# Kernel optimization log

Hardware: AMD Instinct MI355X
Metric: run time of the kernel (lower is better)

The kernel has to match this reference:

```python
import jax, jax.numpy as jnp
import numpy as np

B, C, M, H, K, V, Fdim = 2, 2048, 1024, 16, 64, 64, 4096
EPS = 1e-5


def layer_norm(x, g, b):
    mu = jnp.mean(x, axis=-1, keepdims=True)
    var = jnp.mean((x - mu) ** 2, axis=-1, keepdims=True)
    return (x - mu) * jax.lax.rsqrt(var + EPS) * g + b


def mha(kvinput, qinput, wq, wk, wv, wo, masked):
    # kvinput/qinput: [b,c,m]; wq/wk: [h,m,k]; wv: [h,m,v]; wo: [h,v,m]
    kval = jnp.einsum('bcm,hmk->bhck', kvinput, wk)
    qval = jnp.einsum('bcm,hmk->bhck', qinput, wq)
    vval = jnp.einsum('bcm,hmv->bhcv', kvinput, wv)
    # logits: c indexes keys, d indexes queries (faithful to original)
    alogit = jnp.einsum('bhck,bhdk->bhcd', kval, qval)
    if masked:
        side = alogit.shape[2]
        # triu INCLUDING diagonal, added before scaling (faithful quirk)
        mask = jnp.triu(jnp.full((side, side), -100.0, dtype=alogit.dtype))
        alogit = alogit + mask
    scale = 1.0 / np.sqrt(wq.shape[-1]).astype(np.float32)
    att = jax.nn.softmax(alogit * scale, axis=2)  # normalize over keys c
    pre = jnp.einsum('bhcd,bhcv->bhdv', att, vval)
    return jnp.einsum('bhdv,hvm->bdm', pre, wo)


def setup_inputs() -> dict:
    key = jax.random.key(0)
    ks = jax.random.split(key, 14)
    d = {
        'enc_out': jax.random.normal(ks[0], (B, C, M), jnp.float32),
        'x': jax.random.normal(ks[1], (B, C, M), jnp.float32),
        # masked self-attention params
        'wq1': jax.random.normal(ks[2], (H, M, K), jnp.float32),
        'wk1': jax.random.normal(ks[3], (H, M, K), jnp.float32),
        'wv1': jax.random.normal(ks[4], (H, M, V), jnp.float32),
        'wo1': jax.random.normal(ks[5], (H, V, M), jnp.float32),
        'g1': jnp.ones((M,), jnp.float32), 'b1': jnp.zeros((M,), jnp.float32),
        # cross-attention params
        'wq2': jax.random.normal(ks[6], (H, M, K), jnp.float32),
        'wk2': jax.random.normal(ks[7], (H, M, K), jnp.float32),
        'wv2': jax.random.normal(ks[8], (H, M, V), jnp.float32),
        'wo2': jax.random.normal(ks[9], (H, V, M), jnp.float32),
        'g2': jnp.ones((M,), jnp.float32), 'b2': jnp.zeros((M,), jnp.float32),
        # FFN params
        'fw1': jax.random.normal(ks[10], (M, Fdim), jnp.float32),
        'fb1': jnp.zeros((Fdim,), jnp.float32),
        'fw2': jax.random.normal(ks[11], (Fdim, M), jnp.float32),
        'fb2': jnp.zeros((M,), jnp.float32),
        'g3': jnp.ones((M,), jnp.float32), 'b3': jnp.zeros((M,), jnp.float32),
    }
    return d


def reference(enc_out, x, wq1, wk1, wv1, wo1, g1, b1,
              wq2, wk2, wv2, wo2, g2, b2,
              fw1, fb1, fw2, fb2, g3, b3):
    att1 = mha(x, x, wq1, wk1, wv1, wo1, masked=True)
    n1 = layer_norm(x + att1, g1, b1)
    att2 = mha(enc_out, n1, wq2, wk2, wv2, wo2, masked=False)
    n2 = layer_norm(n1 + att2, g2, b2)
    ff = jnp.einsum('bcf,fm->bcm', jax.nn.relu(jnp.einsum('bcm,mf->bcf', n2, fw1) + fb1), fw2) + fb2
    return layer_norm(n2 + ff, g3, b3)
```

## Files before the change

### kernel.cpp

```cpp
#include <hip/hip_runtime.h>
#include <math.h>

#define B_ 2
#define C_ 2048
#define M_ 1024
#define H_ 16
#define KV_ 64
#define F_ 4096

typedef __attribute__((ext_vector_type(8))) __bf16 bf16x8;
typedef __attribute__((ext_vector_type(4))) float f32x4;
typedef unsigned short u16;

#if defined(__has_builtin)
#if __has_builtin(__builtin_amdgcn_mfma_f64_16x16x4f64)
#define HAVE_MFMA64 1
#endif
#endif
#ifndef HAVE_MFMA64
#define HAVE_MFMA64 0
#endif

#if HAVE_MFMA64
typedef __attribute__((ext_vector_type(4))) double f64x4;
#endif

__device__ __forceinline__ float bf2f(u16 u) {
    union { unsigned int i; float f; } x; x.i = ((unsigned int)u) << 16; return x.f;
}
__device__ __forceinline__ u16 f2bf(float f) {
    union { float f; unsigned int i; } x; x.f = f;
    unsigned int r = x.i + 0x7fffu + ((x.i >> 16) & 1u);
    return (u16)(r >> 16);
}
__device__ __forceinline__ float ldflag(const void* p, size_t i, int isf) {
    return isf ? ((const float*)p)[i] : bf2f(((const u16*)p)[i]);
}

__device__ __forceinline__ double blockReduceSumD(double v, double* red, int tid) {
#pragma unroll
    for (int off = 32; off > 0; off >>= 1) v += __shfl_down(v, off, 64);
    if ((tid & 63) == 0) red[tid >> 6] = v;
    __syncthreads();
    v = red[0] + red[1] + red[2] + red[3];
    __syncthreads();
    return v;
}

__global__ void detect_dtype(const unsigned int* __restrict__ w, int* __restrict__ flags) {
    __shared__ int cnt[256];
    int t = threadIdx.x, c = 0;
    for (int i = t; i < 2048; i += 256) {
        unsigned int e = (w[i] >> 7) & 0xffu;
        if (e >= 140u || (e > 0u && e < 91u)) c++;
    }
    cnt[t] = c; __syncthreads();
    for (int s = 128; s > 0; s >>= 1) { if (t < s) cnt[t] += cnt[t + s]; __syncthreads(); }
    if (t == 0) flags[0] = (cnt[0] > 300) ? 1 : 0;
}

__device__ __forceinline__ float sAval(int m, int k) { return (float)(((m * 5 + k * 3) % 7) - 3); }
__device__ __forceinline__ float sBval(int k, int n) { return (float)(((k * 11 + n * 2) % 5) - 2); }
__device__ __forceinline__ float sQval(int m, int k) { return (float)(((m * 3 + k * 7) % 9) - 4); }
__device__ __forceinline__ float sKval(int c, int k) { return (float)(((c * 5 + k * 2) % 8) - 3); }

__global__ __launch_bounds__(256) void calibrate(int* __restrict__ cal) {
#if HAVE_MFMA64
    __shared__ int ctab[64][12];
    __shared__ int s_ok, s_bad;
    __shared__ float Ast[32][65], Bs[32][65];
    __shared__ float Qv[64][65], Kv[64][65];
    const int t = threadIdx.x;
    if (t == 0) { s_ok = 0; s_bad = 0; }
    __syncthreads();
    if (t < 64) {
        const int l = t;
        f64x4 z = {0.0, 0.0, 0.0, 0.0};
        f64x4 p1 = __builtin_amdgcn_mfma_f64_16x16x4f64(1.0, (double)l, z, 0, 0, 0);
        f64x4 p2 = __builtin_amdgcn_mfma_f64_16x16x4f64((double)l, 1.0, z, 0, 0, 0);
        int ok = 1, bFam = 0, aFam = 0;
        int colD[4], rowD[4];
#pragma unroll
        for (int r = 0; r < 4; r++) {
            double pv = p1[r];
            int f = 0, n = 0;
            if (pv >= 0.0 && pv <= 4096.0) {
                long long vi = (long long)(pv + 0.5);
                if (vi >= 96 && vi <= 156 && ((vi - 96) & 3) == 0) { f = 1; n = (int)((vi - 96) >> 2); }
                else if (vi >= 6 && vi <= 246 && ((vi - 6) & 15) == 0) { f = 2; n = (int)((vi - 6) >> 4); }
            }
            if (f == 0) ok = 0;
            if (r == 0) bFam = f; else if (f != bFam) ok = 0;
            colD[r] = n;
            pv = p2[r]; f = 0; n = 0;
            if (pv >= 0.0 && pv <= 4096.0) {
                long long wi = (long long)(pv + 0.5);
                if (wi >= 96 && wi <= 156 && ((wi - 96) & 3) == 0) { f = 1; n = (int)((wi - 96) >> 2); }
                else if (wi >= 6 && wi <= 246 && ((wi - 6) & 15) == 0) { f = 2; n = (int)((wi - 6) >> 4); }
            }
            if (f == 0) ok = 0;
            if (r == 0) aFam = f; else if (f != aFam) ok = 0;
            rowD[r] = n;
        }
        if (colD[1] != colD[0] || colD[2] != colD[0] || colD[3] != colD[0]) ok = 0;
        int rm = (1 << rowD[0]) | (1 << rowD[1]) | (1 << rowD[2]) | (1 << rowD[3]);
        if (__popc(rm) != 4) ok = 0;
        int cm = 1 << colD[0];
#pragma unroll
        for (int off = 1; off < 16; off <<= 1) {
#pragma unroll
            for (int r = 0; r < 4; r++)
                if (__shfl_xor(rowD[r], off, 64) != rowD[r]) ok = 0;
            cm |= __shfl_xor(cm, off, 64);
        }
        if (cm != 0xffff) ok = 0;
        const int am = (aFam == 2) ? (l >> 2) : (l & 15);
        const int ak = (aFam == 2) ? (l & 3) : (l >> 4);
        const int bn = (bFam == 2) ? (l >> 2) : (l & 15);
        const int bk = (bFam == 2) ? (l & 3) : (l >> 4);
        {
            double a3 = (double)sAval(am, ak);
            double b3 = (double)sBval(bk, bn);
            f64x4 p3 = __builtin_amdgcn_mfma_f64_16x16x4f64(a3, b3, z, 0, 0, 0);
#pragma unroll
            for (int r = 0; r < 4; r++) {
                double ref = 0.0;
                for (int k2 = 0; k2 < 4; k2++)
                    ref += (double)sAval(rowD[r], k2) * (double)sBval(k2, colD[0]);
                if (p3[r] != ref) ok = 0;
            }
        }
        unsigned long long bb = __ballot(ok != 0);
        ctab[l][0] = am; ctab[l][1] = ak; ctab[l][2] = bn; ctab[l][3] = bk;
        ctab[l][4] = colD[0];
        ctab[l][5] = rowD[0]; ctab[l][6] = rowD[1]; ctab[l][7] = rowD[2]; ctab[l][8] = rowD[3];
        ctab[l][9] = 0; ctab[l][10] = 0; ctab[l][11] = 0;
        if (l == 0) s_ok = (bb == ~0ull) ? 1 : 0;
    }
    __syncthreads();
    for (int i = t; i < 32 * 64; i += 256) {
        int k2 = i >> 6, m2 = i & 63;
        Ast[k2][m2] = sAval(m2, k2);
        Bs[k2][m2] = sBval(k2, m2);
    }
    for (int i = t; i < 64 * 64; i += 256) {
        int r2 = i >> 6, c2 = i & 63;
        Qv[r2][c2] = sQval(r2, c2);
        Kv[r2][c2] = sKval(r2, c2);
    }
    __syncthreads();
    if (s_ok) {
        const int w = t >> 6;
        const int* cl = ctab[t & 63];
        const int am = cl[0], ak2 = cl[1], bn2 = cl[2], bk2 = cl[3], cD = cl[4];
        const int rd[4] = {cl[5], cl[6], cl[7], cl[8]};
        int ok = 1;
        {
            f64x4 acc4[4] = { {0,0,0,0},{0,0,0,0},{0,0,0,0},{0,0,0,0} };
#pragma unroll
            for (int ks = 0; ks < 8; ks++) {
                double ad = (double)Ast[4 * ks + ak2][16 * w + am];
#pragma unroll
                for (int nt = 0; nt < 4; nt++) {
                    double bd = (double)Bs[4 * ks + bk2][16 * nt + bn2];
                    acc4[nt] = __builtin_amdgcn_mfma_f64_16x16x4f64(ad, bd, acc4[nt], 0, 0, 0);
                }
            }
#pragma unroll
            for (int nt = 0; nt < 4; nt++)
#pragma unroll
                for (int i = 0; i < 4; i++) {
                    int row = 16 * w + rd[i], col = 16 * nt + cD;
                    double ref = 0.0;
                    for (int k2 = 0; k2 < 32; k2++)
                        ref += (double)sAval(row, k2) * (double)sBval(k2, col);
                    if (acc4[nt][i] != ref) ok = 0;
                }
        }
        {
            double aqv[16];
#pragma unroll
            for (int ks = 0; ks < 16; ks++)
                aqv[ks] = (double)Qv[16 * w + am][4 * ks + ak2];
            f64x4 S[4] = { {0,0,0,0},{0,0,0,0},{0,0,0,0},{0,0,0,0} };
#pragma unroll
            for (int ks = 0; ks < 16; ks++) {
#pragma unroll
                for (int nt = 0; nt < 4; nt++) {
                    double bd = (double)Kv[16 * nt + bn2][4 * ks + bk2];
                    S[nt] = __builtin_amdgcn_mfma_f64_16x16x4f64(aqv[ks], bd, S[nt], 0, 0, 0);
                }
            }
#pragma unroll
            for (int nt = 0; nt < 4; nt++)
#pragma unroll
                for (int i = 0; i < 4; i++) {
                    int row = 16 * w + rd[i], col = 16 * nt + cD;
                    double ref = 0.0;
                    for (int k2 = 0; k2 < 64; k2++)
                        ref += (double)sQval(row, k2) * (double)sKval(col, k2);
                    if (S[nt][i] != ref) ok = 0;
                }
        }
        if (!ok) s_bad = 1;
    }
    __syncthreads();
    if (t < 64) {
#pragma unroll
        for (int j = 0; j < 12; j++) cal[16 + t * 12 + j] = ctab[t][j];
    }
    if (t == 0) cal[0] = (s_ok && !s_bad) ? 1 : 0;
#else
    if (threadIdx.x == 0) cal[0] = 0;
#endif
}

__global__ __launch_bounds__(256) void v_to_bf16t(
    const float* __restrict__ vv, u16* __restrict__ hi, u16* __restrict__ lo)
{
    __shared__ float Ls[64][65];
    const int bh = blockIdx.y, c0 = blockIdx.x * 64;
    const int t = threadIdx.x;
    const int c = t >> 2, vb = (t & 3) * 16;
    const float* src = vv + ((size_t)bh * C_ + c0 + c) * KV_ + vb;
#pragma unroll
    for (int i = 0; i < 4; i++) {
        float4 p = *(const float4*)(src + 4 * i);
        Ls[vb + 4*i + 0][c] = p.x;
        Ls[vb + 4*i + 1][c] = p.y;
        Ls[vb + 4*i + 2][c] = p.z;
        Ls[vb + 4*i + 3][c] = p.w;
    }
    __syncthreads();
#pragma unroll
    for (int it = 0; it < 2; it++) {
        int idx = t + 256 * it;
        int v = idx >> 3, ch = idx & 7;
        u16 h8[8], l8[8];
#pragma unroll
        for (int j = 0; j < 8; j++) {
            float x = Ls[v][ch * 8 + j];
            h8[j] = f2bf(x);
            l8[j] = f2bf(x - bf2f(h8[j]));
        }
        size_t off = ((size_t)bh * KV_ + v) * C_ + c0 + ch * 8;
        int4 hp, lp;
        hp.x = (int)((unsigned)h8[0] | ((unsigned)h8[1] << 16));
        hp.y = (int)((unsigned)h8[2] | ((unsigned)h8[3] << 16));
        hp.z = (int)((unsigned)h8[4] | ((unsigned)h8[5] << 16));
        hp.w = (int)((unsigned)h8[6] | ((unsigned)h8[7] << 16));
        lp.x = (int)((unsigned)l8[0] | ((unsigned)l8[1] << 16));
        lp.y = (int)((unsigned)l8[2] | ((unsigned)l8[3] << 16));
        lp.z = (int)((unsigned)l8[4] | ((unsigned)l8[5] << 16));
        lp.w = (int)((unsigned)l8[6] | ((unsigned)l8[7] << 16));
        *(int4*)(hi + off) = hp;
        *(int4*)(lo + off) = lp;
    }
}

template<int AMODE>
__global__ __launch_bounds__(256) void proj_qk64(
    const void* __restrict__ Ab, const void* __restrict__ Bb,
    float* __restrict__ Cb, const int* __restrict__ flags,
    const int* __restrict__ cal,
    int N, int Kd, long long a_bstr, long long b_hstr, long long c_zstr, int NH)
{
    const int isf = flags[0];
    const int isfA = (AMODE == 1) ? 1 : isf;
    __shared__ float Ast[32][65];
    __shared__ float Bs[32][65];
    const int t = threadIdx.x;
    const int m0 = blockIdx.x * 64, n0 = blockIdx.y * 64;
    const int zb = blockIdx.z / NH, zh = blockIdx.z % NH;
    const size_t aoff = (size_t)zb * a_bstr, boff = (size_t)zh * b_hstr;
    const size_t czoff = (size_t)blockIdx.z * c_zstr;
    const int ar = t >> 2, ak = (t & 3) * 8;
    const int bk = t >> 3, bn = (t & 7) * 8;
    const int cok = cal[0];

#if HAVE_MFMA64
    if (cok) {
        const int* cl = cal + 16 + (t & 63) * 12;
        const int am = cl[0], ak2 = cl[1], bn2 = cl[2], bk2 = cl[3], cD = cl[4];
        const int rd[4] = {cl[5], cl[6], cl[7], cl[8]};
        const int w = t >> 6;
        f64x4 acc4[4] = { {0,0,0,0},{0,0,0,0},{0,0,0,0},{0,0,0,0} };
        for (int k0 = 0; k0 < Kd; k0 += 32) {
            float av[8];
            {
                size_t off = aoff + (size_t)(m0 + ar) * Kd + k0 + ak;
                if (isfA) {
                    const float* ap = (const float*)Ab + off;
                    float4 p0 = *(const float4*)ap, p1 = *((const float4*)ap + 1);
                    av[0]=p0.x; av[1]=p0.y; av[2]=p0.z; av[3]=p0.w;
                    av[4]=p1.x; av[5]=p1.y; av[6]=p1.z; av[7]=p1.w;
                } else {
                    const u16* ap = (const u16*)Ab + off;
                    int4 p = *(const int4*)ap;
                    unsigned int u[4] = {(unsigned)p.x,(unsigned)p.y,(unsigned)p.z,(unsigned)p.w};
#pragma unroll
                    for (int j = 0; j < 4; j++) {
                        av[2*j]   = bf2f((u16)(u[j] & 0xffffu));
                        av[2*j+1] = bf2f((u16)(u[j] >> 16));
                    }
                }
            }
#pragma unroll
            for (int j = 0; j < 8; j++) Ast[ak + j][ar] = av[j];
            float bv[8];
            {
                size_t off = boff + (size_t)(k0 + bk) * N + n0 + bn;
                if (isf) {
                    const float* bp = (const float*)Bb + off;
                    float4 p0 = *(const float4*)bp, p1 = *((const float4*)bp + 1);
                    bv[0]=p0.x; bv[1]=p0.y; bv[2]=p0.z; bv[3]=p0.w;
                    bv[4]=p1.x; bv[5]=p1.y; bv[6]=p1.z; bv[7]=p1.w;
                } else {
                    const u16* bp = (const u16*)Bb + off;
                    int4 p = *(const int4*)bp;
                    unsigned int u[4] = {(unsigned)p.x,(unsigned)p.y,(unsigned)p.z,(unsigned)p.w};
#pragma unroll
                    for (int j = 0; j < 4; j++) {
                        bv[2*j]   = bf2f((u16)(u[j] & 0xffffu));
                        bv[2*j+1] = bf2f((u16)(u[j] >> 16));
                    }
                }
            }
#pragma unroll
            for (int j = 0; j < 8; j++) Bs[bk][bn + j] = bv[j];
            __syncthreads();
#pragma unroll
            for (int ks = 0; ks < 8; ks++) {
                double ad = (double)Ast[4 * ks + ak2][16 * w + am];
#pragma unroll
                for (int nt = 0; nt < 4; nt++) {
                    double bd = (double)Bs[4 * ks + bk2][16 * nt + bn2];
                    acc4[nt] = __builtin_amdgcn_mfma_f64_16x16x4f64(ad, bd, acc4[nt], 0, 0, 0);
                }
            }
            __syncthreads();
        }
#pragma unroll
        for (int nt = 0; nt < 4; nt++)
#pragma unroll
            for (int i = 0; i < 4; i++)
                Cb[czoff + (size_t)(m0 + 16 * w + rd[i]) * N + n0 + 16 * nt + cD] =
                    (float)acc4[nt][i];
        return;
    }
#endif
    double acc[4][4] = {};
    for (int k0 = 0; k0 < Kd; k0 += 32) {
        float av[8];
        {
            size_t off = aoff + (size_t)(m0 + ar) * Kd + k0 + ak;
            if (isfA) {
                const float* ap = (const float*)Ab + off;
                float4 p0 = *(const float4*)ap, p1 = *((const float4*)ap + 1);
                av[0]=p0.x; av[1]=p0.y; av[2]=p0.z; av[3]=p0.w;
                av[4]=p1.x; av[5]=p1.y; av[6]=p1.z; av[7]=p1.w;
            } else {
                const u16* ap = (const u16*)Ab + off;
                int4 p = *(const int4*)ap;
                unsigned int u[4] = {(unsigned)p.x,(unsigned)p.y,(unsigned)p.z,(unsigned)p.w};
#pragma unroll
                for (int j = 0; j < 4; j++) {
                    av[2*j]   = bf2f((u16)(u[j] & 0xffffu));
                    av[2*j+1] = bf2f((u16)(u[j] >> 16));
                }
            }
        }
#pragma unroll
        for (int j = 0; j < 8; j++) Ast[ak + j][ar] = av[j];
        float bv[8];
        {
            size_t off = boff + (size_t)(k0 + bk) * N + n0 + bn;
            if (isf) {
                const float* bp = (const float*)Bb + off;
                float4 p0 = *(const float4*)bp, p1 = *((const float4*)bp + 1);
                bv[0]=p0.x; bv[1]=p0.y; bv[2]=p0.z; bv[3]=p0.w;
                bv[4]=p1.x; bv[5]=p1.y; bv[6]=p1.z; bv[7]=p1.w;
            } else {
                const u16* bp = (const u16*)Bb + off;
                int4 p = *(const int4*)bp;
                unsigned int u[4] = {(unsigned)p.x,(unsigned)p.y,(unsigned)p.z,(unsigned)p.w};
#pragma unroll
                for (int j = 0; j < 4; j++) {
                    bv[2*j]   = bf2f((u16)(u[j] & 0xffffu));
                    bv[2*j+1] = bf2f((u16)(u[j] >> 16));
                }
            }
        }
#pragma unroll
        for (int j = 0; j < 8; j++) Bs[bk][bn + j] = bv[j];
        __syncthreads();
        const int r0 = (t & 15) * 4, c0 = (t >> 4) * 4;
#pragma unroll
        for (int kk = 0; kk < 32; kk++) {
            float4 a4 = *(const float4*)&Ast[kk][r0];
            float4 b4 = *(const float4*)&Bs[kk][c0];
            double a0=a4.x, a1=a4.y, a2=a4.z, a3=a4.w;
            double b0=b4.x, b1=b4.y, b2=b4.z, b3=b4.w;
            acc[0][0] += a0*b0; acc[0][1] += a0*b1; acc[0][2] += a0*b2; acc[0][3] += a0*b3;
            acc[1][0] += a1*b0; acc[1][1] += a1*b1; acc[1][2] += a1*b2; acc[1][3] += a1*b3;
            acc[2][0] += a2*b0; acc[2][1] += a2*b1; acc[2][2] += a2*b2; acc[2][3] += a2*b3;
            acc[3][0] += a3*b0; acc[3][1] += a3*b1; acc[3][2] += a3*b2; acc[3][3] += a3*b3;
        }
        __syncthreads();
    }
    {
        const int r0 = (t & 15) * 4, c0 = (t >> 4) * 4;
#pragma unroll
        for (int i = 0; i < 4; i++)
#pragma unroll
            for (int j = 0; j < 4; j++)
                Cb[czoff + (size_t)(m0 + r0 + i) * N + n0 + c0 + j] = (float)acc[i][j];
    }
}

template<int AMODE, bool RELU, bool BIAS>
__global__ __launch_bounds__(256) void gemm_hilo(
    const void* __restrict__ Ab, const void* __restrict__ Bb,
    float* __restrict__ Cb, const void* __restrict__ bias,
    const int* __restrict__ flags,
    int N, int Kd, long long a_bstr, long long b_hstr, long long c_zstr, int NH)
{
    const int isf = flags[0];
    const int aIsF32 = (AMODE == 1) ? 1 : isf;
    __shared__ u16 a_hi[64][40], a_lo[64][40];
    __shared__ u16 b_hi[64][40], b_lo[64][40];

    const int tid = threadIdx.x;
    const int w = tid >> 6, l = tid & 63;
    const int lq = l & 15, quad = l >> 4;
    const int m0 = blockIdx.x * 64, n0 = blockIdx.y * 64;
    const int zb = blockIdx.z / NH, zh = blockIdx.z % NH;
    const size_t aoff = (size_t)zb * a_bstr, boff = (size_t)zh * b_hstr;

    f32x4 acc[4] = { {0,0,0,0},{0,0,0,0},{0,0,0,0},{0,0,0,0} };
    const int arow = tid >> 2, ac8 = (tid & 3) * 8;
    const int bk = tid >> 3, bn8 = (tid & 7) * 8;

    for (int k0 = 0; k0 < Kd; k0 += 32) {
        {
            size_t off = aoff + (size_t)(m0 + arow) * Kd + k0 + ac8;
            u16 hh[8], ll[8];
            if (aIsF32) {
                const float* ap = (const float*)Ab + off;
                float4 p0 = *(const float4*)ap, p1 = *((const float4*)ap + 1);
                float vv[8] = {p0.x,p0.y,p0.z,p0.w,p1.x,p1.y,p1.z,p1.w};
#pragma unroll
                for (int j = 0; j < 8; j++) {
                    hh[j] = f2bf(vv[j]);
                    ll[j] = f2bf(vv[j] - bf2f(hh[j]));
                }
            } else {
                int4 p = *(const int4*)((const u16*)Ab + off);
                unsigned int u[4] = {(unsigned)p.x,(unsigned)p.y,(unsigned)p.z,(unsigned)p.w};
#pragma unroll
                for (int j = 0; j < 4; j++) {
                    hh[2*j]   = (u16)(u[j] & 0xffffu);
                    hh[2*j+1] = (u16)(u[j] >> 16);
                    ll[2*j] = 0; ll[2*j+1] = 0;
                }
            }
            int4 ph, pl;
            ph.x = (int)((unsigned)hh[0] | ((unsigned)hh[1] << 16));
            ph.y = (int)((unsigned)hh[2] | ((unsigned)hh[3] << 16));
            ph.z = (int)((unsigned)hh[4] | ((unsigned)hh[5] << 16));
            ph.w = (int)((unsigned)hh[6] | ((unsigned)hh[7] << 16));
            pl.x = (int)((unsigned)ll[0] | ((unsigned)ll[1] << 16));
            pl.y = (int)((unsigned)ll[2] | ((unsigned)ll[3] << 16));
            pl.z = (int)((unsigned)ll[4] | ((unsigned)ll[5] << 16));
            pl.w = (int)((unsigned)ll[6] | ((unsigned)ll[7] << 16));
            *(int4*)&a_hi[arow][ac8] = ph;
            *(int4*)&a_lo[arow][ac8] = pl;
        }
        {
            size_t off = boff + (size_t)(k0 + bk) * N + n0 + bn8;
            u16 hh[8], ll[8];
            if (isf) {
                const float* bp = (const float*)Bb + off;
                float4 p0 = *(const float4*)bp, p1 = *((const float4*)bp + 1);
                float vv[8] = {p0.x,p0.y,p0.z,p0.w,p1.x,p1.y,p1.z,p1.w};
#pragma unroll
                for (int j = 0; j < 8; j++) {
                    hh[j] = f2bf(vv[j]);
                    ll[j] = f2bf(vv[j] - bf2f(hh[j]));
                }
            } else {
                int4 p = *(const int4*)((const u16*)Bb + off);
                unsigned int u[4] = {(unsigned)p.x,(unsigned)p.y,(unsigned)p.z,(unsigned)p.w};
#pragma unroll
                for (int j = 0; j < 4; j++) {
                    hh[2*j]   = (u16)(u[j] & 0xffffu);
                    hh[2*j+1] = (u16)(u[j] >> 16);
                    ll[2*j] = 0; ll[2*j+1] = 0;
                }
            }
#pragma unroll
            for (int j = 0; j < 8; j++) {
                b_hi[bn8 + j][bk] = hh[j];
                b_lo[bn8 + j][bk] = ll[j];
            }
        }
        __syncthreads();
        bf16x8 ah = *(bf16x8*)&a_hi[w * 16 + lq][quad * 8];
        bf16x8 al = *(bf16x8*)&a_lo[w * 16 + lq][quad * 8];
#pragma unroll
        for (int nt = 0; nt < 4; nt++) {
            bf16x8 bh = *(bf16x8*)&b_hi[nt * 16 + lq][quad * 8];
            bf16x8 bl = *(bf16x8*)&b_lo[nt * 16 + lq][quad * 8];
            acc[nt] = __builtin_amdgcn_mfma_f32_16x16x32_bf16(ah, bh, acc[nt], 0, 0, 0);
            acc[nt] = __builtin_amdgcn_mfma_f32_16x16x32_bf16(ah, bl, acc[nt], 0, 0, 0);
            acc[nt] = __builtin_amdgcn_mfma_f32_16x16x32_bf16(al, bh, acc[nt], 0, 0, 0);
        }
        __syncthreads();
    }

    const int rowb = m0 + w * 16 + quad * 4;
    const size_t czoff = (size_t)blockIdx.z * c_zstr;
#pragma unroll
    for (int nt = 0; nt < 4; nt++) {
        int col = n0 + nt * 16 + lq;
        float bv = BIAS ? ldflag(bias, col, isf) : 0.0f;
#pragma unroll
        for (int r = 0; r < 4; r++) {
            float val = acc[nt][r] + bv;
            if (RELU) val = fmaxf(val, 0.0f);
            Cb[czoff + (size_t)(rowb + r) * N + col] = val;
        }
    }
}

__global__ __launch_bounds__(256) void attn_fast(
    const float* __restrict__ q, const float* __restrict__ k,
    const u16* __restrict__ vthi, const u16* __restrict__ vtlo,
    float* __restrict__ pre,
    const int* __restrict__ cal, int masked)
{
#if HAVE_MFMA64
    __shared__ float Ks[64][68];
    __shared__ u16 VtH[64][68];
    __shared__ u16 VtL[64][68];
    __shared__ u16 Pslab[4][2][16][68];
    __shared__ float alphaT[64];
    __shared__ float lT[64];

    if (cal[0] == 0) return;

    const int idx = blockIdx.x;
    const int q0 = (idx & (C_ / 64 - 1)) * 64;
    const int h = (idx >> 5) & (H_ - 1);
    const int b = idx >> 9;
    const size_t bh = (size_t)(b * H_ + h);
    const float* Qg = q + (bh * C_ + q0) * KV_;
    const float* Kg = k + bh * C_ * KV_;
    const u16* vthg = vthi + bh * (size_t)KV_ * C_;
    const u16* vtlg = vtlo + bh * (size_t)KV_ * C_;

    const int t = threadIdx.x;
    const int* cl = cal + 16 + (t & 63) * 12;
    const int am = cl[0], ak2 = cl[1], bn2 = cl[2], bk2 = cl[3], cD = cl[4];
    const int rdv[4] = {cl[5], cl[6], cl[7], cl[8]};
    const int w = t >> 6, l15 = t & 15, g = (t >> 4) & 3;
    const int srow = t >> 2, sc = (t & 3) * 16;

    {
        const float* src = Qg + (size_t)srow * KV_ + sc;
#pragma unroll
        for (int i = 0; i < 4; i++)
            *(float4*)&Ks[srow][sc + 4 * i] = *(const float4*)(src + 4 * i);
    }
    __syncthreads();
    double aq[16];
#pragma unroll
    for (int ks = 0; ks < 16; ks++)
        aq[ks] = (double)Ks[16 * w + am][4 * ks + ak2];

    f32x4 acc[4] = { {0,0,0,0},{0,0,0,0},{0,0,0,0},{0,0,0,0} };
    float mreg[4] = {-3.0e38f, -3.0e38f, -3.0e38f, -3.0e38f};
    float lreg[4] = {0.0f, 0.0f, 0.0f, 0.0f};

    for (int kt = 0; kt < 32; kt++) {
        const int c0 = kt * 64;
        __syncthreads();
        {
            const float* ksrc = Kg + (size_t)(c0 + srow) * KV_ + sc;
#pragma unroll
            for (int i = 0; i < 4; i++)
                *(float4*)&Ks[srow][sc + 4 * i] = *(const float4*)(ksrc + 4 * i);
        }
#pragma unroll
        for (int it = 0; it < 4; it++) {
            int idx2 = t + 256 * it;
            int arr = idx2 >> 9, rem = idx2 & 511;
            int vrow = rem >> 3, ch = rem & 7;
            const u16* gsrc = (arr ? vtlg : vthg) + (size_t)vrow * C_ + c0 + ch * 8;
            u16* dst = (arr ? &VtL[vrow][ch * 8] : &VtH[vrow][ch * 8]);
            int4 d = *(const int4*)gsrc;
            *(int2*)dst = make_int2(d.x, d.y);
            *(int2*)(dst + 4) = make_int2(d.z, d.w);
        }
        __syncthreads();

        f64x4 S[4] = { {0,0,0,0},{0,0,0,0},{0,0,0,0},{0,0,0,0} };
#pragma unroll
        for (int ks = 0; ks < 16; ks++) {
#pragma unroll
            for (int nt = 0; nt < 4; nt++) {
                double bd = (double)Ks[16 * nt + bn2][4 * ks + bk2];
                S[nt] = __builtin_amdgcn_mfma_f64_16x16x4f64(aq[ks], bd, S[nt], 0, 0, 0);
            }
        }
        if (masked) {
#pragma unroll
            for (int nt = 0; nt < 4; nt++) {
                const int cg = c0 + 16 * nt + cD;
#pragma unroll
                for (int i = 0; i < 4; i++)
                    if (cg <= q0 + 16 * w + rdv[i]) S[nt][i] -= 100.0;
            }
        }
        float tm[4];
#pragma unroll
        for (int i = 0; i < 4; i++)
            tm[i] = fmaxf(fmaxf((float)S[0][i], (float)S[1][i]),
                          fmaxf((float)S[2][i], (float)S[3][i]));
#pragma unroll
        for (int off = 1; off < 16; off <<= 1)
#pragma unroll
            for (int i = 0; i < 4; i++)
                tm[i] = fmaxf(tm[i], __shfl_xor(tm[i], off, 64));
        float alpha[4];
#pragma unroll
        for (int i = 0; i < 4; i++) {
            const float mo = mreg[i];
            const float mn = fmaxf(mo, tm[i]);
            alpha[i] = (mo < -1.0e37f) ? 0.0f : __expf(0.125f * (mo - mn));
            mreg[i] = mn;
        }
        if (l15 == 0) {
#pragma unroll
            for (int i = 0; i < 4; i++) alphaT[16 * w + rdv[i]] = alpha[i];
        }
        float ts[4] = {0.0f, 0.0f, 0.0f, 0.0f};
#pragma unroll
        for (int nt = 0; nt < 4; nt++) {
#pragma unroll
            for (int i = 0; i < 4; i++) {
                float p = __expf((float)(0.125 * (S[nt][i] - (double)mreg[i])));
                ts[i] += p;
                u16 ph = f2bf(p);
                u16 pl = f2bf(p - bf2f(ph));
                Pslab[w][0][rdv[i]][16 * nt + cD] = ph;
                Pslab[w][1][rdv[i]][16 * nt + cD] = pl;
            }
        }
#pragma unroll
        for (int off = 1; off < 16; off <<= 1)
#pragma unroll
            for (int i = 0; i < 4; i++)
                ts[i] += __shfl_xor(ts[i], off, 64);
#pragma unroll
        for (int i = 0; i < 4; i++)
            lreg[i] = lreg[i] * alpha[i] + ts[i];

        __builtin_amdgcn_sched_barrier(0);
        asm volatile("s_waitcnt lgkmcnt(0)" ::: "memory");
        __builtin_amdgcn_sched_barrier(0);

        float af[4];
#pragma unroll
        for (int i = 0; i < 4; i++) af[i] = alphaT[16 * w + 4 * g + i];
#pragma unroll
        for (int nt = 0; nt < 4; nt++)
#pragma unroll
            for (int i = 0; i < 4; i++) acc[nt][i] *= af[i];

        union F8 { struct { int2 a, b; } p; bf16x8 v; };
#pragma unroll
        for (int ks2 = 0; ks2 < 2; ks2++) {
            const u16* pa = &Pslab[w][0][l15][8 * g + 32 * ks2];
            const u16* pb = &Pslab[w][1][l15][8 * g + 32 * ks2];
            F8 pah, pal;
            pah.p.a = *(const int2*)pa; pah.p.b = *(const int2*)(pa + 4);
            pal.p.a = *(const int2*)pb; pal.p.b = *(const int2*)(pb + 4);
#pragma unroll
            for (int nt = 0; nt < 4; nt++) {
                const u16* vh = &VtH[16 * nt + l15][8 * g + 32 * ks2];
                const u16* vl = &VtL[16 * nt + l15][8 * g + 32 * ks2];
                F8 vbh, vbl;
                vbh.p.a = *(const int2*)vh; vbh.p.b = *(const int2*)(vh + 4);
                vbl.p.a = *(const int2*)vl; vbl.p.b = *(const int2*)(vl + 4);
                acc[nt] = __builtin_amdgcn_mfma_f32_16x16x32_bf16(pah.v, vbh.v, acc[nt], 0, 0, 0);
                acc[nt] = __builtin_amdgcn_mfma_f32_16x16x32_bf16(pah.v, vbl.v, acc[nt], 0, 0, 0);
                acc[nt] = __builtin_amdgcn_mfma_f32_16x16x32_bf16(pal.v, vbh.v, acc[nt], 0, 0, 0);
            }
        }
    }
    if (l15 == 0) {
#pragma unroll
        for (int i = 0; i < 4; i++) lT[16 * w + rdv[i]] = lreg[i];
    }
    __builtin_amdgcn_sched_barrier(0);
    asm volatile("s_waitcnt lgkmcnt(0)" ::: "memory");
    __builtin_amdgcn_sched_barrier(0);
#pragma unroll
    for (int i = 0; i < 4; i++) {
        const float li = lT[16 * w + 4 * g + i];
        const size_t rbase = (((size_t)b * C_ + q0 + 16 * w + 4 * g + i) * H_ + h) * KV_;
#pragma unroll
        for (int nt = 0; nt < 4; nt++)
            pre[rbase + 16 * nt + l15] = acc[nt][i] / li;
    }
#endif
}

__global__ __launch_bounds__(256) void attn_legacy(
    const float* __restrict__ q, const float* __restrict__ k,
    const float* __restrict__ v, float* __restrict__ pre,
    const int* __restrict__ cal, int masked)
{
    __shared__ float Qs[64][68];
    __shared__ float KPs[64][68];
    __shared__ float Vs[64][68];
    __shared__ float redm[64][17];
    __shared__ float redl[64][17];
    __shared__ float mrow[64], lrow[64], arow[64];

    if (cal[0] != 0) return;

    const int idx = blockIdx.x;
    const int q0 = (idx & (C_ / 64 - 1)) * 64;
    const int h = (idx >> 5) & (H_ - 1);
    const int b = idx >> 9;
    const size_t bh = (size_t)(b * H_ + h);
    const float* Qg = q + (bh * C_ + q0) * KV_;
    const float* Kg = k + bh * C_ * KV_;
    const float* Vg = v + bh * C_ * KV_;
    const int t = threadIdx.x;
    const int tq = t & 15, tc = t >> 4;
    const int srow = t >> 2, scol = (t & 3) * 16;

    {
        const float* src = Qg + (size_t)srow * KV_ + scol;
#pragma unroll
        for (int i = 0; i < 4; i++) {
            float4 p4 = *(const float4*)(src + 4 * i);
            Qs[scol + 4*i + 0][srow] = p4.x;
            Qs[scol + 4*i + 1][srow] = p4.y;
            Qs[scol + 4*i + 2][srow] = p4.z;
            Qs[scol + 4*i + 3][srow] = p4.w;
        }
    }
    if (t < 64) { mrow[t] = -3.0e38f; lrow[t] = 0.0f; }

    float O[4][4] = {};

    for (int kt = 0; kt < 32; kt++) {
        const int c0 = kt * 64;
        __syncthreads();
        {
            const float* ksrc = Kg + (size_t)(c0 + srow) * KV_ + scol;
#pragma unroll
            for (int i = 0; i < 4; i++) {
                float4 p4 = *(const float4*)(ksrc + 4 * i);
                KPs[scol + 4*i + 0][srow] = p4.x;
                KPs[scol + 4*i + 1][srow] = p4.y;
                KPs[scol + 4*i + 2][srow] = p4.z;
                KPs[scol + 4*i + 3][srow] = p4.w;
            }
            const float* vsrc = Vg + (size_t)(c0 + srow) * KV_ + scol;
#pragma unroll
            for (int i = 0; i < 4; i++)
                *(float4*)&Vs[srow][scol + 4 * i] = *(const float4*)(vsrc + 4 * i);
        }
        __syncthreads();

        double Sd[4][4] = {};
#pragma unroll 4
        for (int j = 0; j < 64; j++) {
            float4 qa = *(const float4*)&Qs[j][4 * tq];
            float4 kb = *(const float4*)&KPs[j][4 * tc];
            double qd[4] = {qa.x, qa.y, qa.z, qa.w};
            double kd[4] = {kb.x, kb.y, kb.z, kb.w};
#pragma unroll
            for (int i = 0; i < 4; i++)
#pragma unroll
                for (int jj = 0; jj < 4; jj++)
                    Sd[i][jj] += qd[i] * kd[jj];
        }
        if (masked) {
#pragma unroll
            for (int i = 0; i < 4; i++)
#pragma unroll
                for (int jj = 0; jj < 4; jj++)
                    if (c0 + 4 * tc + jj <= q0 + 4 * tq + i) Sd[i][jj] -= 100.0;
        }
#pragma unroll
        for (int i = 0; i < 4; i++) {
            double mm = fmax(fmax(Sd[i][0], Sd[i][1]), fmax(Sd[i][2], Sd[i][3]));
            redm[4 * tq + i][tc] = (float)mm;
        }
        __syncthreads();
        if (t < 64) {
            float tmv = redm[t][0];
#pragma unroll
            for (int x = 1; x < 16; x++) tmv = fmaxf(tmv, redm[t][x]);
            float mo = mrow[t];
            float mn = fmaxf(mo, tmv);
            arow[t] = (mo < -1.0e37f) ? 0.0f
                       : (float)exp(0.125 * ((double)mo - (double)mn));
            mrow[t] = mn;
        }
        __syncthreads();
#pragma unroll
        for (int i = 0; i < 4; i++) {
            double mn = (double)mrow[4 * tq + i];
            float ls = 0.0f;
#pragma unroll
            for (int jj = 0; jj < 4; jj++) {
                float p = (float)exp(0.125 * (Sd[i][jj] - mn));
                KPs[4 * tc + jj][4 * tq + i] = p;
                ls += p;
            }
            redl[4 * tq + i][tc] = ls;
        }
        __syncthreads();
        if (t < 64) {
            float s = 0.0f;
#pragma unroll
            for (int x = 0; x < 16; x++) s += redl[t][x];
            lrow[t] = lrow[t] * arow[t] + s;
        }
        float al[4];
#pragma unroll
        for (int i = 0; i < 4; i++) al[i] = arow[4 * tq + i];
#pragma unroll
        for (int i = 0; i < 4; i++)
#pragma unroll
            for (int jj = 0; jj < 4; jj++) O[i][jj] *= al[i];
#pragma unroll 4
        for (int c = 0; c < 64; c++) {
            float4 pa = *(const float4*)&KPs[c][4 * tq];
            float4 vb = *(const float4*)&Vs[c][4 * tc];
            float pd[4] = {pa.x, pa.y, pa.z, pa.w};
            float vd[4] = {vb.x, vb.y, vb.z, vb.w};
#pragma unroll
            for (int i = 0; i < 4; i++)
#pragma unroll
                for (int jj = 0; jj < 4; jj++)
                    O[i][jj] += pd[i] * vd[jj];
        }
    }
    __syncthreads();
#pragma unroll
    for (int i = 0; i < 4; i++) {
        float li = lrow[4 * tq + i];
        float4 o4;
        o4.x = O[i][0] / li; o4.y = O[i][1] / li;
        o4.z = O[i][2] / li; o4.w = O[i][3] / li;
        *(float4*)&pre[(((size_t)b * C_ + q0 + 4 * tq + i) * H_ + h) * KV_ + 4 * tc] = o4;
    }
}

template<int IN1MODE, int OUTMODE>
__global__ __launch_bounds__(256) void ln_f64(
    const void* __restrict__ in1, const float* __restrict__ in2,
    const void* __restrict__ g, const void* __restrict__ b,
    void* __restrict__ out, const int* __restrict__ flags)
{
    __shared__ double buf[M_];
    __shared__ double red[4];
    const int isf = flags[0];
    const int row = blockIdx.x;
    const size_t base = (size_t)row * M_;
    const int tid = threadIdx.x;
    double s = 0.0;
    for (int i = tid; i < M_; i += 256) {
        double v1 = (IN1MODE == 1) ? (double)((const float*)in1)[base + i]
                                   : (double)ldflag(in1, base + i, isf);
        double val = v1 + (double)in2[base + i];
        buf[i] = val;
        s += val;
    }
    s = blockReduceSumD(s, red, tid);
    const double mu = s * (1.0 / M_);
    double vs = 0.0;
    for (int i = tid; i < M_; i += 256) { double dd = buf[i] - mu; vs += dd * dd; }
    vs = blockReduceSumD(vs, red, tid);
    const double rstd = 1.0 / sqrt(vs * (1.0 / M_) + 1e-5);
    for (int i = tid; i < M_; i += 256) {
        double y = (buf[i] - mu) * rstd * (double)ldflag(g, i, isf) + (double)ldflag(b, i, isf);
        if (OUTMODE == 0) ((float*)out)[base + i] = (float)y;
        else if (isf)     ((float*)out)[base + i] = (float)y;
        else              ((u16*)out)[base + i] = f2bf((float)y);
    }
}

extern "C" void kernel_launch(void* const* d_in, const int* in_sizes, int n_in,
                              void* d_out, int out_size, void* d_ws, size_t ws_size,
                              hipStream_t stream)
{
    const void* enc = d_in[0];
    const void* x   = d_in[1];
    const void* wq1 = d_in[2];
    const void* wk1 = d_in[3];
    const void* wv1 = d_in[4];
    const void* wo1 = d_in[5];
    const void* g1  = d_in[6];
    const void* b1  = d_in[7];
    const void* wq2 = d_in[8];
    const void* wk2 = d_in[9];
    const void* wv2 = d_in[10];
    const void* wo2 = d_in[11];
    const void* g2  = d_in[12];
    const void* b2  = d_in[13];
    const void* fw1 = d_in[14];
    const void* fb1 = d_in[15];
    const void* fw2 = d_in[16];
    const void* fb2 = d_in[17];
    const void* g3  = d_in[18];
    const void* b3  = d_in[19];

    int* fl = (int*)d_ws;
    int* cal = fl + 16;
    const size_t NQ = (size_t)B_ * C_ * M_;
    float* S0 = (float*)((char*)d_ws + 4096);
    float* S1 = S0 + NQ;
    float* S2 = S1 + NQ;
    float* S3 = S2 + NQ;
    float* S4 = S3 + NQ;
    float* q = S0, *kk = S1, *vv = S2, *pre = S3, *attout = S1, *n1 = S4, *n2 = S4;
    float* h1 = S0;
    float* ff = (float*)d_out;
    u16* vt1h = (u16*)S4;
    u16* vt1l = vt1h + (size_t)B_ * H_ * KV_ * C_;
    u16* vt2h = (u16*)d_out;
    u16* vt2l = vt2h + (size_t)B_ * H_ * KV_ * C_;

    dim3 blk(256);
    dim3 gproj(C_ / 64, KV_ / 64, B_ * H_);
    dim3 gout(B_ * C_ / 64, M_ / 64, 1);
    dim3 gffn1(B_ * C_ / 64, F_ / 64, 1);
    dim3 gffn2(B_ * C_ / 64, M_ / 64, 1);
    dim3 gattn(B_ * H_ * (C_ / 64));
    dim3 gvt(C_ / 64, B_ * H_);
    dim3 gln(B_ * C_);
    const long long AB = (long long)C_ * M_, BH = (long long)M_ * KV_, CZ = (long long)C_ * KV_;

    detect_dtype<<<1, 256, 0, stream>>>((const unsigned int*)wq1, fl);
    calibrate<<<1, 256, 0, stream>>>(cal);

    proj_qk64<0><<<gproj, blk, 0, stream>>>(x, wq1, q,  fl, cal, KV_, M_, AB, BH, CZ, H_);
    proj_qk64<0><<<gproj, blk, 0, stream>>>(x, wk1, kk, fl, cal, KV_, M_, AB, BH, CZ, H_);
    gemm_hilo<0,false,false><<<gproj, blk, 0, stream>>>(x, wv1, vv, nullptr, fl, KV_, M_, AB, BH, CZ, H_);
    v_to_bf16t<<<gvt, blk, 0, stream>>>(vv, vt1h, vt1l);
    attn_fast<<<gattn, blk, 0, stream>>>(q, kk, vt1h, vt1l, pre, cal, 1);
    attn_legacy<<<gattn, blk, 0, stream>>>(q, kk, vv, pre, cal, 1);
    gemm_hilo<1,false,false><<<gout, blk, 0, stream>>>(pre, wo1, attout, nullptr, fl, M_, M_, 0, 0, 0, 1);
    ln_f64<0, 0><<<gln, blk, 0, stream>>>(x, attout, g1, b1, n1, fl);

    proj_qk64<1><<<gproj, blk, 0, stream>>>(n1, wq2, q,  fl, cal, KV_, M_, AB, BH, CZ, H_);
    proj_qk64<0><<<gproj, blk, 0, stream>>>(enc, wk2, kk, fl, cal, KV_, M_, AB, BH, CZ, H_);
    gemm_hilo<0,false,false><<<gproj, blk, 0, stream>>>(enc, wv2, vv, nullptr, fl, KV_, M_, AB, BH, CZ, H_);
    v_to_bf16t<<<gvt, blk, 0, stream>>>(vv, vt2h, vt2l);
    attn_fast<<<gattn, blk, 0, stream>>>(q, kk, vt2h, vt2l, pre, cal, 0);
    attn_legacy<<<gattn, blk, 0, stream>>>(q, kk, vv, pre, cal, 0);
    gemm_hilo<1,false,false><<<gout, blk, 0, stream>>>(pre, wo2, attout, nullptr, fl, M_, M_, 0, 0, 0, 1);
    ln_f64<1, 0><<<gln, blk, 0, stream>>>(n1, attout, g2, b2, n2, fl);

    gemm_hilo<1,true,true><<<gffn1, blk, 0, stream>>>(n2, fw1, h1, fb1, fl, F_, M_, 0, 0, 0, 1);
    gemm_hilo<1,false,true><<<gffn2, blk, 0, stream>>>(h1, fw2, ff, fb2, fl, M_, F_, 0, 0, 0, 1);
    ln_f64<1, 1><<<gln, blk, 0, stream>>>(n2, ff, g3, b3, d_out, fl);
}
```

Baseline: 2.903 ms.

## Swizzle GEMM B-tile LDS columns and vectorize layernorm loads/stores

Result: faster. 2.527 ms (-12.9%).

```diff
diff --git a/kernel.cpp b/kernel.cpp
--- a/kernel.cpp
+++ b/kernel.cpp
@@ -440,6 +440,7 @@
     f32x4 acc[4] = { {0,0,0,0},{0,0,0,0},{0,0,0,0},{0,0,0,0} };
     const int arow = tid >> 2, ac8 = (tid & 3) * 8;
     const int bk = tid >> 3, bn8 = (tid & 7) * 8;
+    const int bflip = (tid & 3) << 3;
 
     for (int k0 = 0; k0 < Kd; k0 += 32) {
         {
@@ -498,10 +499,11 @@
                     ll[2*j] = 0; ll[2*j+1] = 0;
                 }
             }
+            const int bkc = bk ^ bflip;
 #pragma unroll
             for (int j = 0; j < 8; j++) {
-                b_hi[bn8 + j][bk] = hh[j];
-                b_lo[bn8 + j][bk] = ll[j];
+                b_hi[bn8 + j][bkc] = hh[j];
+                b_lo[bn8 + j][bkc] = ll[j];
             }
         }
         __syncthreads();
@@ -509,8 +511,9 @@
         bf16x8 al = *(bf16x8*)&a_lo[w * 16 + lq][quad * 8];
 #pragma unroll
         for (int nt = 0; nt < 4; nt++) {
-            bf16x8 bh = *(bf16x8*)&b_hi[nt * 16 + lq][quad * 8];
-            bf16x8 bl = *(bf16x8*)&b_lo[nt * 16 + lq][quad * 8];
+            const int bcol = (quad * 8) ^ (((2 * nt + (lq >> 3)) & 3) << 3);
+            bf16x8 bh = *(bf16x8*)&b_hi[nt * 16 + lq][bcol];
+            bf16x8 bl = *(bf16x8*)&b_lo[nt * 16 + lq][bcol];
             acc[nt] = __builtin_amdgcn_mfma_f32_16x16x32_bf16(ah, bh, acc[nt], 0, 0, 0);
             acc[nt] = __builtin_amdgcn_mfma_f32_16x16x32_bf16(ah, bl, acc[nt], 0, 0, 0);
             acc[nt] = __builtin_amdgcn_mfma_f32_16x16x32_bf16(al, bh, acc[nt], 0, 0, 0);
@@ -877,13 +880,24 @@
     const int row = blockIdx.x;
     const size_t base = (size_t)row * M_;
     const int tid = threadIdx.x;
+    const bool vec = (IN1MODE == 1) || isf;
     double s = 0.0;
-    for (int i = tid; i < M_; i += 256) {
-        double v1 = (IN1MODE == 1) ? (double)((const float*)in1)[base + i]
-                                   : (double)ldflag(in1, base + i, isf);
-        double val = v1 + (double)in2[base + i];
-        buf[i] = val;
-        s += val;
+    if (vec) {
+        const float4 a4 = *(const float4*)((const float*)in1 + base + tid * 4);
+        const float4 b4 = *(const float4*)(in2 + base + tid * 4);
+        double v0 = (double)a4.x + (double)b4.x;
+        double v1 = (double)a4.y + (double)b4.y;
+        double v2 = (double)a4.z + (double)b4.z;
+        double v3 = (double)a4.w + (double)b4.w;
+        buf[tid] = v0; buf[tid + 256] = v1; buf[tid + 512] = v2; buf[tid + 768] = v3;
+        s = ((v0 + v1) + (v2 + v3));
+    } else {
+        for (int i = tid; i < M_; i += 256) {
+            double v1 = (double)ldflag(in1, base + i, isf);
+            double val = v1 + (double)in2[base + i];
+            buf[i] = val;
+            s += val;
+        }
     }
     s = blockReduceSumD(s, red, tid);
     const double mu = s * (1.0 / M_);
@@ -891,11 +905,27 @@
     for (int i = tid; i < M_; i += 256) { double dd = buf[i] - mu; vs += dd * dd; }
     vs = blockReduceSumD(vs, red, tid);
     const double rstd = 1.0 / sqrt(vs * (1.0 / M_) + 1e-5);
-    for (int i = tid; i < M_; i += 256) {
-        double y = (buf[i] - mu) * rstd * (double)ldflag(g, i, isf) + (double)ldflag(b, i, isf);
-        if (OUTMODE == 0) ((float*)out)[base + i] = (float)y;
-        else if (isf)     ((float*)out)[base + i] = (float)y;
-        else              ((u16*)out)[base + i] = f2bf((float)y);
+    if (vec) {
+        double y0 = (buf[tid      ] - mu) * rstd * (double)ldflag(g, 4*tid+0, isf) + (double)ldflag(b, 4*tid+0, isf);
+        double y1 = (buf[tid + 256] - mu) * rstd * (double)ldflag(g, 4*tid+1, isf) + (double)ldflag(b, 4*tid+1, isf);
+        double y2 = (buf[tid + 512] - mu) * rstd * (double)ldflag(g, 4*tid+2, isf) + (double)ldflag(b, 4*tid+2, isf);
+        double y3 = (buf[tid + 768] - mu) * rstd * (double)ldflag(g, 4*tid+3, isf) + (double)ldflag(b, 4*tid+3, isf);
+        if (OUTMODE == 0 || isf) {
+            float4 o4;
+            o4.x = (float)y0; o4.y = (float)y1; o4.z = (float)y2; o4.w = (float)y3;
+            *(float4*)((float*)out + base + tid * 4) = o4;
+        } else {
+            u16* op = (u16*)out + base + tid * 4;
+            op[0] = f2bf((float)y0); op[1] = f2bf((float)y1);
+            op[2] = f2bf((float)y2); op[3] = f2bf((float)y3);
+        }
+    } else {
+        for (int i = tid; i < M_; i += 256) {
+            double y = (buf[i] - mu) * rstd * (double)ldflag(g, i, isf) + (double)ldflag(b, i, isf);
+            if (OUTMODE == 0) ((float*)out)[base + i] = (float)y;
+            else if (isf)     ((float*)out)[base + i] = (float)y;
+            else              ((u16*)out)[base + i] = f2bf((float)y);
+        }
     }
 }
 
```
